# Performance work log

Hardware: AMD Instinct MI355X
Metric: run time of the kernel (lower is better)

The kernel has to match this reference:

```python
import jax, jax.numpy as jnp
import numpy as np

EMBED_DIM = 1024
NUM_HEADS = 16
HEAD_DIM = EMBED_DIM // NUM_HEADS
BATCH = 2
SEQ = 2048


def setup_inputs() -> dict:
    key = jax.random.key(0)
    k_x, k_wi, k_bi, k_wo, k_bo = jax.random.split(key, 5)
    scale_in = 1.0 / np.sqrt(EMBED_DIM)
    x = jax.random.normal(k_x, (BATCH, SEQ, EMBED_DIM), dtype=jnp.float32)
    # nn.Linear stores weight [out, in]; we keep [in, out] for x @ W.
    w_in = jax.random.uniform(k_wi, (EMBED_DIM, 3 * EMBED_DIM), jnp.float32, -scale_in, scale_in)
    b_in = jax.random.uniform(k_bi, (3 * EMBED_DIM,), jnp.float32, -scale_in, scale_in)
    w_out = jax.random.uniform(k_wo, (EMBED_DIM, EMBED_DIM), jnp.float32, -scale_in, scale_in)
    b_out = jax.random.uniform(k_bo, (EMBED_DIM,), jnp.float32, -scale_in, scale_in)
    return {"x": x, "w_in": w_in, "b_in": b_in, "w_out": w_out, "b_out": b_out}


def reference(x, w_in, b_in, w_out, b_out):
    B, S, E = x.shape
    H, D = NUM_HEADS, HEAD_DIM
    inp = x @ w_in + b_in                       # [B,S,3E]
    que, key, val = jnp.split(inp, 3, axis=-1)  # each [B,S,E]
    que = que.reshape(B, S, H, D)
    key = key.reshape(B, S, H, D)
    val = val.reshape(B, S, H, D)
    scores = jnp.einsum('bshd,brhd->bhsr', que, key) * (1.0 / np.sqrt(D))
    weights = jax.nn.softmax(scores, axis=-1)   # [B,H,S,S]
    attn = jnp.einsum('bhsr,brhd->bshd', weights, val).reshape(B, S, E)
    return attn @ w_out + b_out
```

## Files before the change

kernel.cpp:

```cpp
#include <hip/hip_runtime.h>


typedef __bf16 bf16x8 __attribute__((ext_vector_type(8)));
typedef float  f32x4  __attribute__((ext_vector_type(4)));
typedef float  f32x16 __attribute__((ext_vector_type(16)));
typedef short  s16x4  __attribute__((ext_vector_type(4)));
typedef short  s16x8  __attribute__((ext_vector_type(8)));

__device__ __forceinline__ unsigned short f2b(float f) {
  unsigned u = __float_as_uint(f);
  unsigned r = u + 0x7fffu + ((u >> 16) & 1u);
  return (unsigned short)(r >> 16);
}

__device__ __forceinline__ unsigned cvt_pk_bf16(float a, float b) {
#if defined(__HIP_DEVICE_COMPILE__)
  unsigned r;
  asm("v_cvt_pk_bf16_f32 %0, %1, %2" : "=v"(r) : "v"(a), "v"(b));
  return r;
#else
  return (unsigned)f2b(a) | ((unsigned)f2b(b) << 16);
#endif
}

__device__ __forceinline__ void permlane32_swap(unsigned& a, unsigned& b) {
#if defined(__HIP_DEVICE_COMPILE__)
  asm("v_permlane32_swap_b32 %0, %1" : "+v"(a), "+v"(b));
#endif
}

__device__ __forceinline__ void gl_lds16(const void* g, void* l) {
  __builtin_amdgcn_global_load_lds(
      (__attribute__((address_space(1))) void*)g,
      (__attribute__((address_space(3))) void*)l, 16, 0, 0);
}

__device__ __forceinline__ void transpose_cast_body(
    const float* __restrict__ in, unsigned short* __restrict__ out,
    int R, int C, int bx, int by, int tid, float tile[64][65]) {
  int r0 = by * 64, c0 = bx * 64;
#pragma unroll
  for (int p = 0; p < 16; p++) {
    int i = tid + p * 256;
    int ri = i >> 6, ci = i & 63;
    tile[ri][ci] = in[(size_t)(r0 + ri) * C + c0 + ci];
  }
  __syncthreads();
#pragma unroll
  for (int p = 0; p < 16; p++) {
    int i = tid + p * 256;
    int ci = i >> 6, ri = i & 63;
    out[(size_t)(c0 + ci) * R + r0 + ri] = f2b(tile[ri][ci]);
  }
}

__global__ __launch_bounds__(256) void prep_kernel(
    const float* __restrict__ x, unsigned short* __restrict__ xb,
    const float* __restrict__ w_in, unsigned short* __restrict__ wint,
    const float* __restrict__ w_out, unsigned short* __restrict__ woutt) {
  __shared__ float tile[64][65];
  int bid = blockIdx.x, tid = threadIdx.x;
  if (bid < 4096) {
    int i = bid * 256 + tid;
    float4 v = ((const float4*)x)[i];
    ushort4 o;
    o.x = f2b(v.x); o.y = f2b(v.y); o.z = f2b(v.z); o.w = f2b(v.w);
    ((ushort4*)xb)[i] = o;
  } else if (bid < 4864) {
    int l = bid - 4096;
    transpose_cast_body(w_in, wint, 1024, 3072, l % 48, l / 48, tid, tile);
  } else {
    int l = bid - 4864;
    transpose_cast_body(w_out, woutt, 1024, 1024, l % 16, l / 16, tid, tile);
  }
}

__global__ __launch_bounds__(256) void vt_transpose_kernel(
    const unsigned short* __restrict__ qkv, unsigned short* __restrict__ vt) {
  __shared__ unsigned short tile[64][65];
  int bid = blockIdx.x;
  int st = bid & 31, h = (bid >> 5) & 15, b = bid >> 9;
  int s0 = st * 64;
  int tid = threadIdx.x;
  const unsigned short* src = qkv + (size_t)(b * 2048 + s0) * 3072 + 2048 + h * 64;
#pragma unroll
  for (int p = 0; p < 16; p++) {
    int i = tid + p * 256;
    int sr = i >> 6, d = i & 63;
    tile[sr][d] = src[(size_t)sr * 3072 + d];
  }
  __syncthreads();
  unsigned short* dst = vt + (size_t)(b * 16 + h) * 64 * 2048 + s0;
#pragma unroll
  for (int p = 0; p < 16; p++) {
    int i = tid + p * 256;
    int dr = i >> 6, sc = i & 63;
    dst[(size_t)dr * 2048 + sc] = tile[sc][dr];
  }
}

__global__ __launch_bounds__(256) void gemm_bt1(
    const unsigned short* __restrict__ A, const unsigned short* __restrict__ Bt,
    const float* __restrict__ bias, unsigned short* __restrict__ Cp,
    int M, int N, int K, int qcols, float qscale) {
  __shared__ __align__(16) unsigned short As[128 * 32];
  __shared__ __align__(16) unsigned short Bs[128 * 32];
  int tid = threadIdx.x;
  int wave = tid >> 6, lane = tid & 63;
  int m_l = lane & 15, quad = lane >> 4;
  int wm = (wave >> 1) * 64, wn = (wave & 1) * 64;
  int row = tid >> 2, kp = (tid & 3) << 3;
  const unsigned short* ag = A + (size_t)(blockIdx.y * 128 + row) * K + kp;
  const unsigned short* bg = Bt + (size_t)(blockIdx.x * 128 + row) * K + kp;
  unsigned short* asw = As + wave * 512;
  unsigned short* bsw = Bs + wave * 512;
  f32x4 acc[4][4] = {};
  for (int k0 = 0; k0 < K; k0 += 32) {
    __syncthreads();
    gl_lds16(ag + k0, asw);
    gl_lds16(ag + (size_t)64 * K + k0, asw + 2048);
    gl_lds16(bg + k0, bsw);
    gl_lds16(bg + (size_t)64 * K + k0, bsw + 2048);
    __syncthreads();
    bf16x8 af[4], bf[4];
#pragma unroll
    for (int i = 0; i < 4; i++)
      af[i] = *(const bf16x8*)&As[(wm + i * 16 + m_l) * 32 + quad * 8];
#pragma unroll
    for (int j = 0; j < 4; j++)
      bf[j] = *(const bf16x8*)&Bs[(wn + j * 16 + m_l) * 32 + quad * 8];
#pragma unroll
    for (int i = 0; i < 4; i++)
#pragma unroll
      for (int j = 0; j < 4; j++)
        acc[i][j] = __builtin_amdgcn_mfma_f32_16x16x32_bf16(af[i], bf[j], acc[i][j], 0, 0, 0);
  }
  float bv[4];
#pragma unroll
  for (int j = 0; j < 4; j++) bv[j] = bias[blockIdx.x * 128 + wn + j * 16 + m_l];
#pragma unroll
  for (int i = 0; i < 4; i++) {
    int m = blockIdx.y * 128 + wm + i * 16 + quad * 4;
#pragma unroll
    for (int j = 0; j < 4; j++) {
      int n = blockIdx.x * 128 + wn + j * 16 + m_l;
      float sc = (n < qcols) ? qscale : 1.0f;
#pragma unroll
      for (int r = 0; r < 4; r++) {
        float v = (acc[i][j][r] + bv[j]) * sc;
        Cp[(size_t)(m + r) * N + n] = f2b(v);
      }
    }
  }
}

__global__ __launch_bounds__(256) void gemm_bt2(
    const unsigned short* __restrict__ A, const unsigned short* __restrict__ Bt,
    const float* __restrict__ bias, float* __restrict__ Cp, int M, int N, int K) {
  __shared__ __align__(16) unsigned short As[128 * 32];
  __shared__ __align__(16) unsigned short Bs[64 * 32];
  int tid = threadIdx.x;
  int wave = tid >> 6, lane = tid & 63;
  int m_l = lane & 15, quad = lane >> 4;
  int wm = (wave >> 1) * 64, wn = (wave & 1) * 32;
  int row = tid >> 2, kp = (tid & 3) << 3;
  const unsigned short* ag = A + (size_t)(blockIdx.y * 128 + row) * K + kp;
  const unsigned short* bg = Bt + (size_t)(blockIdx.x * 64 + row) * K + kp;
  unsigned short* asw = As + wave * 512;
  unsigned short* bsw = Bs + wave * 512;
  f32x4 acc[4][2] = {};
  for (int k0 = 0; k0 < K; k0 += 32) {
    __syncthreads();
    gl_lds16(ag + k0, asw);
    gl_lds16(ag + (size_t)64 * K + k0, asw + 2048);
    gl_lds16(bg + k0, bsw);
    __syncthreads();
    bf16x8 af[4], bf[2];
#pragma unroll
    for (int i = 0; i < 4; i++)
      af[i] = *(const bf16x8*)&As[(wm + i * 16 + m_l) * 32 + quad * 8];
#pragma unroll
    for (int j = 0; j < 2; j++)
      bf[j] = *(const bf16x8*)&Bs[(wn + j * 16 + m_l) * 32 + quad * 8];
#pragma unroll
    for (int i = 0; i < 4; i++)
#pragma unroll
      for (int j = 0; j < 2; j++)
        acc[i][j] = __builtin_amdgcn_mfma_f32_16x16x32_bf16(af[i], bf[j], acc[i][j], 0, 0, 0);
  }
  float bv[2];
#pragma unroll
  for (int j = 0; j < 2; j++) bv[j] = bias[blockIdx.x * 64 + wn + j * 16 + m_l];
#pragma unroll
  for (int i = 0; i < 4; i++) {
    int m = blockIdx.y * 128 + wm + i * 16 + quad * 4;
#pragma unroll
    for (int j = 0; j < 2; j++) {
      int n = blockIdx.x * 64 + wn + j * 16 + m_l;
#pragma unroll
      for (int r = 0; r < 4; r++)
        Cp[(size_t)(m + r) * N + n] = acc[i][j][r] + bv[j];
    }
  }
}

__global__ __launch_bounds__(512, 4) void attn_kernel(
    const unsigned short* __restrict__ qkv, const unsigned short* __restrict__ vt,
    unsigned short* __restrict__ aout) {
  __shared__ __align__(16) unsigned short smem[24576];
  unsigned short* Qs  = smem;
  unsigned short* Ks  = smem + 8192;
  unsigned short* Vts = smem + 16384;

  int bid = blockIdx.x;
  int qt = bid & 15, h = (bid >> 4) & 15, b = bid >> 8;
  int tid = threadIdx.x, wave = tid >> 6, lane = tid & 63;
  int l31 = lane & 31, hi = lane >> 5, l7 = lane & 7;
  int w03 = wave & 3;
  int koff = (wave >> 2) * 64;
  int q0 = qt * 128;
  const unsigned short* qb = qkv + (size_t)b * 2048 * 3072 + h * 64;
  const unsigned short* kb = qb + 1024;
  const unsigned short* vtb = vt + (size_t)(b * 16 + h) * 64 * 2048;

  int srow = tid >> 3;
  int sd0 = ((tid & 7) ^ (srow & 7)) * 8;
  int dv = tid >> 4;
  int sv = tid & 15;
  int gv = (sv & 8) | ((sv & 7) ^ (dv & 7));

#pragma unroll
  for (int p = 0; p < 2; p++)
    gl_lds16(qb + (size_t)(q0 + p * 64 + srow) * 3072 + sd0, Qs + p * 4096 + wave * 512);
  __syncthreads();

  bf16x8 qf[4];
  int qrow = (w03 * 32 + l31) * 64;
#pragma unroll
  for (int ks = 0; ks < 4; ks++)
    qf[ks] = *(const bf16x8*)&Qs[qrow + ((2 * ks + hi) ^ l7) * 8];

  union { s16x8 s; bf16x8 v; } onesu;
  onesu.s = (s16x8){0x3F80, 0x3F80, 0x3F80, 0x3F80, 0x3F80, 0x3F80, 0x3F80, 0x3F80};

  f32x16 oacc[2] = {};
  f32x16 lacc = {};

  for (int kt = 0; kt < 2048; kt += 128) {
    __syncthreads();
    gl_lds16(kb + (size_t)(kt + srow) * 3072 + sd0, Ks + wave * 512);
    gl_lds16(kb + (size_t)(kt + 64 + srow) * 3072 + sd0, Ks + 4096 + wave * 512);
    gl_lds16(vtb + (size_t)dv * 2048 + kt + gv * 8, Vts + wave * 512);
    gl_lds16(vtb + (size_t)(32 + dv) * 2048 + kt + gv * 8, Vts + 4096 + wave * 512);
    __syncthreads();

#pragma unroll
    for (int tt = 0; tt < 2; tt++) {
      f32x16 sacc = {};
#pragma unroll
      for (int ks = 0; ks < 4; ks++) {
        bf16x8 kf = *(const bf16x8*)&Ks[(koff + tt * 32 + l31) * 64 + ((2 * ks + hi) ^ l7) * 8];
        sacc = __builtin_amdgcn_mfma_f32_32x32x16_bf16(kf, qf[ks], sacc, 0, 0, 0);
      }
      float pv[16];
#pragma unroll
      for (int i = 0; i < 16; i++) pv[i] = __builtin_exp2f(sacc[i]);
#pragma unroll
      for (int g = 0; g < 2; g++) {
        unsigned a0 = cvt_pk_bf16(pv[8 * g + 0], pv[8 * g + 1]);
        unsigned a1 = cvt_pk_bf16(pv[8 * g + 2], pv[8 * g + 3]);
        unsigned b0 = cvt_pk_bf16(pv[8 * g + 4], pv[8 * g + 5]);
        unsigned b1 = cvt_pk_bf16(pv[8 * g + 6], pv[8 * g + 7]);
        permlane32_swap(a0, b0);
        permlane32_swap(a1, b1);
        union { unsigned u[4]; bf16x8 v; } pf;
        pf.u[0] = a0; pf.u[1] = a1; pf.u[2] = b0; pf.u[3] = b1;
        lacc = __builtin_amdgcn_mfma_f32_32x32x16_bf16(onesu.v, pf.v, lacc, 0, 0, 0);
        int kc = tt * 2 + g;
#pragma unroll
        for (int dt = 0; dt < 2; dt++) {
          bf16x8 vf = *(const bf16x8*)&Vts[(dt * 32 + l31) * 128 +
                                           ((koff >> 3) | ((kc * 2 + hi) ^ l7)) * 8];
          oacc[dt] = __builtin_amdgcn_mfma_f32_32x32x16_bf16(vf, pf.v, oacc[dt], 0, 0, 0);
        }
      }
    }
  }

  __syncthreads();
  float* red = (float*)smem;
  float* lpred = red + 8192;
  if (wave >= 4) {
    float* basep = red + w03 * 2048;
#pragma unroll
    for (int dt = 0; dt < 2; dt++)
#pragma unroll
      for (int r = 0; r < 4; r++) {
        f32x4 c4 = {oacc[dt][4 * r + 0], oacc[dt][4 * r + 1],
                    oacc[dt][4 * r + 2], oacc[dt][4 * r + 3]};
        ((f32x4*)basep)[lane * 8 + ((dt * 4 + r) ^ (lane & 7))] = c4;
      }
    lpred[w03 * 64 + lane] = lacc[0];
  }
  __syncthreads();
  if (wave < 4) {
    float* basep = red + w03 * 2048;
#pragma unroll
    for (int dt = 0; dt < 2; dt++)
#pragma unroll
      for (int r = 0; r < 4; r++) {
        f32x4 c4 = ((f32x4*)basep)[lane * 8 + ((dt * 4 + r) ^ (lane & 7))];
        oacc[dt][4 * r + 0] += c4[0];
        oacc[dt][4 * r + 1] += c4[1];
        oacc[dt][4 * r + 2] += c4[2];
        oacc[dt][4 * r + 3] += c4[3];
      }
    float rl = 1.0f / (lacc[0] + lpred[w03 * 64 + lane]);

    unsigned short* ob = aout + (size_t)(b * 2048 + q0 + w03 * 32 + l31) * 1024 + h * 64;
#pragma unroll
    for (int dt = 0; dt < 2; dt++)
#pragma unroll
      for (int rq = 0; rq < 4; rq++) {
        union { uint2 u; ushort4 w; } pk;
        pk.u.x = cvt_pk_bf16(oacc[dt][4 * rq + 0] * rl, oacc[dt][4 * rq + 1] * rl);
        pk.u.y = cvt_pk_bf16(oacc[dt][4 * rq + 2] * rl, oacc[dt][4 * rq + 3] * rl);
        *(ushort4*)&ob[dt * 32 + rq * 8 + hi * 4] = pk.w;
      }
  }
}

extern "C" void kernel_launch(void* const* d_in, const int* in_sizes, int n_in,
                              void* d_out, int out_size, void* d_ws, size_t ws_size,
                              hipStream_t stream) {
  (void)in_sizes; (void)n_in; (void)out_size; (void)ws_size;
  const float* x     = (const float*)d_in[0];
  const float* w_in  = (const float*)d_in[1];
  const float* b_in  = (const float*)d_in[2];
  const float* w_out = (const float*)d_in[3];
  const float* b_out = (const float*)d_in[4];
  char* ws = (char*)d_ws;
  unsigned short* xb    = (unsigned short*)(ws + 0);
  unsigned short* wint  = (unsigned short*)(ws + 8388608);
  unsigned short* woutt = (unsigned short*)(ws + 14680064);
  unsigned short* qkv   = (unsigned short*)(ws + 16777216);
  unsigned short* vt    = (unsigned short*)(ws + 41943040);
  unsigned short* attn  = (unsigned short*)(ws + 50331648);
  float* out = (float*)d_out;

  const float QSCALE = 0.125f * 1.44269504088896f;

  prep_kernel<<<5120, 256, 0, stream>>>(x, xb, w_in, wint, w_out, woutt);
  gemm_bt1<<<dim3(24, 32), 256, 0, stream>>>(xb, wint, b_in, qkv, 4096, 3072, 1024,
                                             1024, QSCALE);
  vt_transpose_kernel<<<1024, 256, 0, stream>>>(qkv, vt);
  attn_kernel<<<512, 512, 0, stream>>>(qkv, vt, attn);
  gemm_bt2<<<dim3(16, 32), 256, 0, stream>>>(attn, woutt, b_out, out, 4096, 1024, 1024);
}
```

Measured before the change: 202.8 us.

## Double-buffer K/V tiles in LDS to overlap loads with attention compute

Splits the single K/V LDS staging area into two buffers and prefetches the next 128-key tile while the current one is being computed. This removes the load-then-wait barrier at the start of every key tile. Wave priority is also raised around the MFMA compute blocks. LDS per block grows from about 48KB to 80KB, which lowers the number of blocks that can be resident per CU, though the grid size may already limit residency.

```diff
diff --git a/kernel.cpp b/kernel.cpp
--- a/kernel.cpp
+++ b/kernel.cpp
@@ -207,10 +207,12 @@
 __global__ __launch_bounds__(512, 4) void attn_kernel(
     const unsigned short* __restrict__ qkv, const unsigned short* __restrict__ vt,
     unsigned short* __restrict__ aout) {
-  __shared__ __align__(16) unsigned short smem[24576];
+  __shared__ __align__(16) unsigned short smem[40960];
   unsigned short* Qs  = smem;
-  unsigned short* Ks  = smem + 8192;
-  unsigned short* Vts = smem + 16384;
+  unsigned short* Ks0 = smem + 8192;
+  unsigned short* Ks1 = smem + 16384;
+  unsigned short* Vt0 = smem + 24576;
+  unsigned short* Vt1 = smem + 32768;
 
   int bid = blockIdx.x;
   int qt = bid & 15, h = (bid >> 4) & 15, b = bid >> 8;
@@ -229,9 +231,17 @@
   int sv = tid & 15;
   int gv = (sv & 8) | ((sv & 7) ^ (dv & 7));
 
+  auto stageKV = [&](unsigned short* Kb, unsigned short* Vb, int kt) {
+    gl_lds16(kb + (size_t)(kt + srow) * 3072 + sd0, Kb + wave * 512);
+    gl_lds16(kb + (size_t)(kt + 64 + srow) * 3072 + sd0, Kb + 4096 + wave * 512);
+    gl_lds16(vtb + (size_t)dv * 2048 + kt + gv * 8, Vb + wave * 512);
+    gl_lds16(vtb + (size_t)(32 + dv) * 2048 + kt + gv * 8, Vb + 4096 + wave * 512);
+  };
+
 #pragma unroll
   for (int p = 0; p < 2; p++)
     gl_lds16(qb + (size_t)(q0 + p * 64 + srow) * 3072 + sd0, Qs + p * 4096 + wave * 512);
+  stageKV(Ks0, Vt0, 0);
   __syncthreads();
 
   bf16x8 qf[4];
@@ -246,20 +256,13 @@
   f32x16 oacc[2] = {};
   f32x16 lacc = {};
 
-  for (int kt = 0; kt < 2048; kt += 128) {
-    __syncthreads();
-    gl_lds16(kb + (size_t)(kt + srow) * 3072 + sd0, Ks + wave * 512);
-    gl_lds16(kb + (size_t)(kt + 64 + srow) * 3072 + sd0, Ks + 4096 + wave * 512);
-    gl_lds16(vtb + (size_t)dv * 2048 + kt + gv * 8, Vts + wave * 512);
-    gl_lds16(vtb + (size_t)(32 + dv) * 2048 + kt + gv * 8, Vts + 4096 + wave * 512);
-    __syncthreads();
-
+  auto computeKV = [&](const unsigned short* Kb, const unsigned short* Vb) {
 #pragma unroll
     for (int tt = 0; tt < 2; tt++) {
       f32x16 sacc = {};
 #pragma unroll
       for (int ks = 0; ks < 4; ks++) {
-        bf16x8 kf = *(const bf16x8*)&Ks[(koff + tt * 32 + l31) * 64 + ((2 * ks + hi) ^ l7) * 8];
+        bf16x8 kf = *(const bf16x8*)&Kb[(koff + tt * 32 + l31) * 64 + ((2 * ks + hi) ^ l7) * 8];
         sacc = __builtin_amdgcn_mfma_f32_32x32x16_bf16(kf, qf[ks], sacc, 0, 0, 0);
       }
       float pv[16];
@@ -279,15 +282,27 @@
         int kc = tt * 2 + g;
 #pragma unroll
         for (int dt = 0; dt < 2; dt++) {
-          bf16x8 vf = *(const bf16x8*)&Vts[(dt * 32 + l31) * 128 +
-                                           ((koff >> 3) | ((kc * 2 + hi) ^ l7)) * 8];
+          bf16x8 vf = *(const bf16x8*)&Vb[(dt * 32 + l31) * 128 +
+                                          ((koff >> 3) | ((kc * 2 + hi) ^ l7)) * 8];
           oacc[dt] = __builtin_amdgcn_mfma_f32_32x32x16_bf16(vf, pf.v, oacc[dt], 0, 0, 0);
         }
       }
     }
-  }
-
-  __syncthreads();
+  };
+
+  for (int kt = 0; kt < 2048; kt += 256) {
+    stageKV(Ks1, Vt1, kt + 128);
+    __builtin_amdgcn_s_setprio(1);
+    computeKV(Ks0, Vt0);
+    __builtin_amdgcn_s_setprio(0);
+    __syncthreads();
+    if (kt + 256 < 2048) stageKV(Ks0, Vt0, kt + 256);
+    __builtin_amdgcn_s_setprio(1);
+    computeKV(Ks1, Vt1);
+    __builtin_amdgcn_s_setprio(0);
+    __syncthreads();
+  }
+
   float* red = (float*)smem;
   float* lpred = red + 8192;
   if (wave >= 4) {
```

Result: no change. 200.9 us (-0.9%).
